# Kernel optimization log

Hardware: AMD Instinct MI355X
Metric: run time of the kernel (lower is better)

The kernel has to match this reference:

```python
import jax, jax.numpy as jnp
import numpy as np

# Module hyperparameters (from init_kwargs)
H, F = 8, 32            # num_heads, attention_filters
RY, RX = 3, 3           # spatial_radius
PH, PW = 2 * RY + 1, 2 * RX + 1
S = PH * PW             # patch_size = 49
HF = H * F


def setup_inputs() -> dict:
    key = jax.random.key(0)
    ks = jax.random.split(key, 6)
    B, Y, X, C = 4, 64, 64, 256
    x = jax.random.normal(ks[0], (B, Y, X, C), jnp.float32)
    # 1x1 conv kernels == dense matrices over the channel dim (no bias)
    Wq = jax.random.normal(ks[1], (C, HF), jnp.float32) / np.sqrt(C)
    Wk = jax.random.normal(ks[2], (C, HF), jnp.float32) / np.sqrt(C)
    Wv = jax.random.normal(ks[3], (C, HF), jnp.float32) / np.sqrt(C)
    Wo = jax.random.normal(ks[4], (HF, C), jnp.float32) / np.sqrt(HF)
    pos_emb = jax.random.normal(ks[5], (S, HF), jnp.float32) * 0.02
    return {"x": x, "Wq": Wq, "Wk": Wk, "Wv": Wv, "Wo": Wo, "pos_emb": pos_emb}


def reference(x, Wq, Wk, Wv, Wo, pos_emb):
    B, Y, X, C = x.shape
    dtype = x.dtype
    # 1x1 conv projections
    Q = x @ Wq                       # (B,Y,X,HF)
    K = x @ Wk
    V = x @ Wv
    # clipped patch centers (borders reuse interior patches)
    cy = jnp.clip(jnp.arange(Y), RY, Y - RY - 1)   # (Y,)
    cx = jnp.clip(jnp.arange(X), RX, X - RX - 1)   # (X,)
    # query relative-position indices within its patch
    qy = jnp.arange(Y) - cy + RY
    qx = jnp.arange(X) - cx + RX
    qidx = qy[:, None] * PW + qx[None, :]          # (Y,X) in [0,S)
    Q = Q + pos_emb[qidx]                          # add query pos embedding (HF)
    Q = Q.reshape(B, Y, X, H, F)
    K = K.reshape(B, Y, X, H, F)
    V = V.reshape(B, Y, X, H, F)
    cy_g, cx_g = jnp.meshgrid(cy, cx, indexing="ij")  # (Y,X)
    scale = jnp.asarray(1.0 / np.sqrt(F), dtype)
    NEG = jnp.asarray(-1e9, dtype)
    m = jnp.full((B, Y, X, H, 1), NEG, dtype)      # running max
    l = jnp.zeros((B, Y, X, H, 1), dtype)          # running sum-exp
    acc = jnp.zeros((B, Y, X, H, F), dtype)        # running value accumulator
    dy_vec = np.arange(-RY, RY + 1)                # within-chunk offsets ('col' mode)
    for dx in range(-RX, RX + 1):                  # chunk loop over columns (7 chunks)
        ny = jnp.clip(cy_g[None, :, :] + dy_vec[:, None, None], 0, Y - 1)  # (PH,Y,X)
        nx = jnp.clip(cx_g[None, :, :] + dx, 0, X - 1)                     # (1,Y,X)
        nx = jnp.broadcast_to(nx, ny.shape)
        sidx = (dy_vec + RY) * PW + (dx + RX)      # (PH,) relative-pos indices
        # gather neighbor K/V: (B,PH,Y,X,H,F)
        Kc = K[:, ny, nx] + pos_emb[sidx].reshape(PH, 1, 1, H, F)
        Vc = V[:, ny, nx]
        sc = jnp.einsum("byxhf,bsyxhf->byxhs", Q, Kc) * scale  # (B,Y,X,H,PH)
        new_m = jnp.maximum(m, sc.max(axis=-1, keepdims=True))
        alpha = jnp.exp(m - new_m)
        p = jnp.exp(sc - new_m)
        l = l * alpha + p.sum(axis=-1, keepdims=True)
        acc = acc * alpha + jnp.einsum("byxhs,bsyxhf->byxhf", p, Vc)
        m = new_m
    out = (acc / (l + 1e-8)).reshape(B, Y, X, HF) @ Wo
    return out
```

## Files before the change

### kernel.cpp

```cpp
#include <hip/hip_runtime.h>
#include <hip/hip_bf16.h>

static constexpr int NPOS = 4 * 64 * 64;
static constexpr int CD   = 256;
#define QSCALE (0.17677669529663687f * 1.4426950408889634f)

typedef __attribute__((ext_vector_type(8))) short bf16x8;
typedef __attribute__((ext_vector_type(4))) float f32x4;

__device__ __forceinline__ float bflo(unsigned int u) { return __uint_as_float(u << 16); }
__device__ __forceinline__ float bfhi(unsigned int u) { return __uint_as_float(u & 0xffff0000u); }

__device__ __forceinline__ unsigned short bfbits(float f) {
    union { __hip_bfloat16 h; unsigned short u; } cv;
    cv.h = __float2bfloat16(f);
    return cv.u;
}
__device__ __forceinline__ unsigned int packbf2(float lo, float hi) {
    union { __hip_bfloat162 h; unsigned int u; } cv;
    cv.h.x = __float2bfloat16(lo);
    cv.h.y = __float2bfloat16(hi);
    return cv.u;
}
__device__ __forceinline__ uint4 pack8(float4 a, float4 b) {
    uint4 u;
    u.x = packbf2(a.x, a.y); u.y = packbf2(a.z, a.w);
    u.z = packbf2(b.x, b.y); u.w = packbf2(b.z, b.w);
    return u;
}
template<int CTRL>
__device__ __forceinline__ float dpp_mov(float v) {
    return __int_as_float(
        __builtin_amdgcn_update_dpp(0, __float_as_int(v), CTRL, 0xF, 0xF, true));
}
template<int IMM>
__device__ __forceinline__ float swz(float v) {
    return __int_as_float(__builtin_amdgcn_ds_swizzle(__float_as_int(v), IMM));
}
__device__ __forceinline__ void async16(void* lds, const void* g) {
    __builtin_amdgcn_global_load_lds(
        (const __attribute__((address_space(1))) unsigned int*)g,
        (__attribute__((address_space(3))) unsigned int*)lds, 16, 0, 0);
}

__global__ __launch_bounds__(256) void convertx_kernel(
    const float* __restrict__ x, unsigned short* __restrict__ xb)
{
    int t = blockIdx.x * 256 + threadIdx.x;
    const float4* s = (const float4*)x + (size_t)t * 2;
    float4 a = s[0], b = s[1];
    ((uint4*)xb)[t] = pack8(a, b);
}

__global__ __launch_bounds__(256) void convert1_kernel(
    const float* __restrict__ Wq, const float* __restrict__ Wk,
    const float* __restrict__ Wv, const float* __restrict__ Wo,
    const float* __restrict__ pe,
    __hip_bfloat16* __restrict__ Wfrag,
    __hip_bfloat16* __restrict__ pebf,
    __hip_bfloat16* __restrict__ Wofrag)
{
    int t = blockIdx.x * 256 + threadIdx.x;
    if (t < 24576) {
        int L = t & 63, ng = (t >> 6) & 7, s = (t >> 9) & 7, T = t >> 12;
        int mat = T >> 1;
        const float* src = (mat == 0) ? Wq : (mat == 1) ? Wk : Wv;
        int ncol  = (T & 1) * 128 + ng * 16 + (L & 15);
        int kbase = s * 32 + (L >> 4) * 8;
        __hip_bfloat16* dst = Wfrag + ((size_t)((T * 8 + s) * 8 + ng) * 64 + L) * 8;
#pragma unroll
        for (int j = 0; j < 8; ++j)
            dst[j] = __float2bfloat16(src[(kbase + j) * 256 + ncol]);
    } else if (t < 26624) {
        int u = t - 24576;
        int L = u & 63, Tn = (u >> 6) & 3, h = u >> 8;
        int s = Tn * 16 + (L & 15);
        int kbase = (L >> 4) * 8;
        __hip_bfloat16* dst = pebf + ((size_t)((h * 4 + Tn) * 64 + L)) * 8;
#pragma unroll
        for (int j = 0; j < 8; ++j) {
            float v = (s < 49) ? pe[s * 256 + h * 32 + kbase + j] * QSCALE : 0.f;
            dst[j] = __float2bfloat16(v);
        }
    } else if (t < 34816) {
        int u = t - 26624;
        int L = u & 63, ng = (u >> 6) & 7, s = (u >> 9) & 7, T = (u >> 12) & 1;
        int ncol  = T * 128 + ng * 16 + (L & 15);
        int kbase = s * 32 + (L >> 4) * 8;
        __hip_bfloat16* dst = Wofrag + ((size_t)((T * 8 + s) * 8 + ng) * 64 + L) * 8;
#pragma unroll
        for (int j = 0; j < 8; ++j)
            dst[j] = __float2bfloat16(Wo[(kbase + j) * 256 + ncol]);
    }
}

__global__ __launch_bounds__(256, 4) void qkv_mfma(
    const unsigned short* __restrict__ xb,
    const __hip_bfloat16* __restrict__ Wfrag,
    const float* __restrict__ pe,
    unsigned short* __restrict__ QA,
    unsigned short* __restrict__ Kd,
    unsigned short* __restrict__ Vt)
{
    __shared__ __align__(16) short As[2][64 * 32];
    const int t = threadIdx.x;
    const int rowbase = blockIdx.x * 64;
    const int g = blockIdx.y;
    const int L = t & 63;
    const int wave = t >> 6;
    const int quad = L >> 4, lrow = L & 15;
    const int T = g * 2 + (wave >> 1);
    const int ngb = (wave & 1) * 4;

    f32x4 acc[4][4];
#pragma unroll
    for (int i = 0; i < 4; ++i)
#pragma unroll
        for (int j = 0; j < 4; ++j) acc[i][j] = (f32x4){0.f, 0.f, 0.f, 0.f};

    const unsigned short* xs = xb + (size_t)(rowbase + (t >> 2)) * CD + (t & 3) * 8;
    short* d0 = &As[0][t * 8];
    short* d1 = &As[1][t * 8];

    async16(d0, xs);
    __syncthreads();

#pragma unroll
    for (int s = 0; s < 8; ++s) {
        if (s < 7) async16((s & 1) ? d0 : d1, xs + (s + 1) * 32);
        bf16x8 bfr[4];
#pragma unroll
        for (int j = 0; j < 4; ++j)
            bfr[j] = *(const bf16x8*)(Wfrag +
                      ((size_t)((T * 8 + s) * 8 + ngb + j) * 64 + L) * 8);
        const short* Ab = As[s & 1];
#pragma unroll
        for (int i = 0; i < 4; ++i) {
            bf16x8 af = *(const bf16x8*)(Ab + (i * 16 + lrow) * 32 + quad * 8);
#pragma unroll
            for (int j = 0; j < 4; ++j)
                acc[i][j] = __builtin_amdgcn_mfma_f32_16x16x32_bf16(af, bfr[j], acc[i][j], 0, 0, 0);
        }
        __syncthreads();
    }

#pragma unroll
    for (int i = 0; i < 4; ++i) {
#pragma unroll
        for (int r = 0; r < 4; ++r) {
            int row = rowbase + i * 16 + quad * 4 + r;
            if (g == 0) {
                int yy = (row >> 6) & 63, xx = row & 63;
                int cy = min(max(yy, 3), 60), cx = min(max(xx, 3), 60);
                int qidx = (yy - cy + 3) * 7 + (xx - cx + 3);
#pragma unroll
                for (int j = 0; j < 4; ++j) {
                    int c = wave * 64 + j * 16 + lrow;
                    QA[(size_t)row * CD + c] = bfbits(acc[i][j][r] + pe[qidx * 256 + c]);
                }
            } else if (g == 1) {
#pragma unroll
                for (int j = 0; j < 4; ++j) {
                    int c = wave * 64 + j * 16 + lrow;
                    Kd[(size_t)row * CD + c] = bfbits(acc[i][j][r] * QSCALE);
                }
            } else {
#pragma unroll
                for (int j = 0; j < 4; ++j) {
                    int c = wave * 64 + j * 16 + lrow;
                    Vt[(size_t)c * 16384 + row + 3] = bfbits(acc[i][j][r]);
                }
            }
        }
    }
}

__global__ __launch_bounds__(256) void attn_mfma(
    unsigned short* QA,
    const unsigned short* __restrict__ Kd,
    const unsigned short* __restrict__ Vt,
    const __hip_bfloat16* __restrict__ pebf)
{
    __shared__ float qpes[4][16 * 64];
    __shared__ __align__(16) unsigned short ps[4][16 * 40];
    const int t = threadIdx.x, w = t >> 6, L = t & 63;
    const int lrow = L & 15, quad = L >> 4;
    const int id = blockIdx.x * 4 + w;
    const int tile = id >> 3, h = id & 7;
    const int pos0 = tile * 16;
    const int x0 = pos0 & 63;
    const int yy = (pos0 >> 6) & 63, bb = pos0 >> 12;
    const int cy = min(max(yy, 3), 60);

    int cxr[4];
#pragma unroll
    for (int r = 0; r < 4; ++r)
        cxr[r] = min(max(x0 + quad * 4 + r, 3), 60) - x0;

    const int kc0 = min(max(x0 - 3 + lrow, 0), 63);
    const int kc1 = min(max(x0 + 13 + lrow, 0), 63);

    const bf16x8 qa = *(const bf16x8*)(QA + (size_t)(pos0 + lrow) * 256 + h * 32 + quad * 8);

    float* qp = qpes[w];
    const f32x4 zero = {0.f, 0.f, 0.f, 0.f};
#pragma unroll
    for (int Tn = 0; Tn < 4; ++Tn) {
        bf16x8 bp = *(const bf16x8*)(pebf + ((size_t)((h * 4 + Tn) * 64 + L)) * 8);
        f32x4 c = __builtin_amdgcn_mfma_f32_16x16x32_bf16(qa, bp, zero, 0, 0, 0);
#pragma unroll
        for (int r = 0; r < 4; ++r)
            qp[(quad * 4 + r) * 64 + Tn * 16 + lrow] = c[r];
    }
    __builtin_amdgcn_s_waitcnt(0xc07f);

    float lacc[4] = {0.f, 0.f, 0.f, 0.f};
    f32x4 o0 = zero, o1 = zero;
    unsigned short* pw = ps[w];
    int rowpos = bb * 4096 + (cy - 3) * 64;

    for (int dy = 0; dy < 7; ++dy, rowpos += 64) {
        const bf16x8 bk0 = *(const bf16x8*)(Kd + (size_t)(rowpos + kc0) * 256 + h * 32 + quad * 8);
        const bf16x8 bk1 = *(const bf16x8*)(Kd + (size_t)(rowpos + kc1) * 256 + h * 32 + quad * 8);
        f32x4 sc0 = __builtin_amdgcn_mfma_f32_16x16x32_bf16(qa, bk0, zero, 0, 0, 0);
        f32x4 sc1 = __builtin_amdgcn_mfma_f32_16x16x32_bf16(qa, bk1, zero, 0, 0, 0);
        const int dy7 = dy * 7;
#pragma unroll
        for (int r = 0; r < 4; ++r) {
            const int i = quad * 4 + r;
            {
                int dx3 = lrow - cxr[r];
                float qpe = qp[i * 64 + dy7 + min(max(dx3, 0), 6)];
                float e = exp2f(sc0[r] + qpe);
                float p = ((unsigned)dx3 <= 6u) ? e : 0.f;
                lacc[r] += p;
                pw[i * 40 + lrow] = bfbits(p);
            }
            {
                int dx3 = 16 + lrow - cxr[r];
                float qpe = qp[i * 64 + dy7 + min(max(dx3, 0), 6)];
                float e = exp2f(sc1[r] + qpe);
                float p = ((unsigned)dx3 <= 6u) ? e : 0.f;
                lacc[r] += p;
                pw[i * 40 + 16 + lrow] = bfbits(p);
            }
        }
        __builtin_amdgcn_s_waitcnt(0xc07f);
        const bf16x8 pa = *(const bf16x8*)(pw + lrow * 40 + quad * 8);
        const bf16x8 bv0 = *(const bf16x8*)(Vt + (size_t)(h * 32 + lrow) * 16384 + rowpos + x0 + quad * 8);
        const bf16x8 bv1 = *(const bf16x8*)(Vt + (size_t)(h * 32 + 16 + lrow) * 16384 + rowpos + x0 + quad * 8);
        o0 = __builtin_amdgcn_mfma_f32_16x16x32_bf16(pa, bv0, o0, 0, 0, 0);
        o1 = __builtin_amdgcn_mfma_f32_16x16x32_bf16(pa, bv1, o1, 0, 0, 0);
    }

#pragma unroll
    for (int r = 0; r < 4; ++r) {
        float v = lacc[r];
        v += dpp_mov<0xB1>(v);
        v += dpp_mov<0x4E>(v);
        v += swz<0x101F>(v);
        v += swz<0x201F>(v);
        const float inv = 1.f / (v + 1e-8f);
        const int row = pos0 + quad * 4 + r;
        QA[(size_t)row * 256 + h * 32 + lrow]      = bfbits(o0[r] * inv);
        QA[(size_t)row * 256 + h * 32 + 16 + lrow] = bfbits(o1[r] * inv);
    }
}

__global__ __launch_bounds__(256, 4) void oproj_mfma(
    const unsigned short* __restrict__ A,
    const __hip_bfloat16* __restrict__ Wofrag,
    float* __restrict__ out)
{
    __shared__ __align__(16) short As[2][32 * 32];
    const int t = threadIdx.x;
    const int rowbase = blockIdx.x * 32;
    const int L = t & 63;
    const int wave = t >> 6;
    const int quad = L >> 4, lrow = L & 15;
    const int T = wave >> 1;
    const int ngb = (wave & 1) * 4;

    f32x4 acc[2][4];
#pragma unroll
    for (int i = 0; i < 2; ++i)
#pragma unroll
        for (int j = 0; j < 4; ++j) acc[i][j] = (f32x4){0.f, 0.f, 0.f, 0.f};

    const unsigned short* asrc = A + (size_t)(rowbase + (t >> 2)) * CD + (t & 3) * 8;
    short* d0 = &As[0][t * 8];
    short* d1 = &As[1][t * 8];

    if (t < 128) async16(d0, asrc);
    __syncthreads();

#pragma unroll
    for (int s = 0; s < 8; ++s) {
        if (s < 7 && t < 128) async16((s & 1) ? d0 : d1, asrc + (s + 1) * 32);
        bf16x8 bfr[4];
#pragma unroll
        for (int j = 0; j < 4; ++j)
            bfr[j] = *(const bf16x8*)(Wofrag +
                      ((size_t)((T * 8 + s) * 8 + ngb + j) * 64 + L) * 8);
        const short* Ab = As[s & 1];
#pragma unroll
        for (int i = 0; i < 2; ++i) {
            bf16x8 af = *(const bf16x8*)(Ab + (i * 16 + lrow) * 32 + quad * 8);
#pragma unroll
            for (int j = 0; j < 4; ++j)
                acc[i][j] = __builtin_amdgcn_mfma_f32_16x16x32_bf16(af, bfr[j], acc[i][j], 0, 0, 0);
        }
        __syncthreads();
    }

#pragma unroll
    for (int i = 0; i < 2; ++i)
#pragma unroll
        for (int r = 0; r < 4; ++r) {
            int row = rowbase + i * 16 + quad * 4 + r;
#pragma unroll
            for (int j = 0; j < 4; ++j) {
                int c = wave * 64 + j * 16 + lrow;
                out[(size_t)row * CD + c] = acc[i][j][r];
            }
        }
}

extern "C" void kernel_launch(void* const* d_in, const int* in_sizes, int n_in,
                              void* d_out, int out_size, void* d_ws, size_t ws_size,
                              hipStream_t stream)
{
    const float* x  = (const float*)d_in[0];
    const float* Wq = (const float*)d_in[1];
    const float* Wk = (const float*)d_in[2];
    const float* Wv = (const float*)d_in[3];
    const float* Wo = (const float*)d_in[4];
    const float* pe = (const float*)d_in[5];
    float* out = (float*)d_out;

    char* ws = (char*)d_ws;
    unsigned short* QA = (unsigned short*)ws;
    unsigned short* Kd = (unsigned short*)(ws + (8u << 20));
    unsigned short* Vt = (unsigned short*)(ws + (16u << 20));
    unsigned short* xb = (unsigned short*)(ws + (24u << 20) + 4096);
    char* fr = ws + (32u << 20) + 8192;
    __hip_bfloat16* Wfrag  = (__hip_bfloat16*)fr;
    __hip_bfloat16* pebf   = (__hip_bfloat16*)(fr + (384u << 10));
    __hip_bfloat16* Wofrag = (__hip_bfloat16*)(fr + (416u << 10));

    convertx_kernel<<<2048, 256, 0, stream>>>(x, xb);
    convert1_kernel<<<136, 256, 0, stream>>>(Wq, Wk, Wv, Wo, pe, Wfrag, pebf, Wofrag);
    qkv_mfma<<<dim3(256, 3), 256, 0, stream>>>(xb, Wfrag, pe, QA, Kd, Vt);
    attn_mfma<<<2048, 256, 0, stream>>>(QA, Kd, Vt, pebf);
    oproj_mfma<<<512, 256, 0, stream>>>(QA, Wofrag, out);
}
```

Before: 138.4 us.

## Merge convert kernels and split V projection with LDS-transposed coalesced stores

Folds the two conversion kernels into one launch. Moves the V projection into its own kernel that stages the transposed output in shared memory, so that Vt writes become contiguous vector stores instead of scattered 2-byte stores. Vt no longer carries a +3 column offset, and the attention kernel's key-window base and V-load offsets shift by 8 to match the new alignment. This trades an extra launch and more LDS use in exchange for coalesced transposed writes.

```diff
diff --git a/kernel.cpp b/kernel.cpp
--- a/kernel.cpp
+++ b/kernel.cpp
@@ -7,9 +7,6 @@
 
 typedef __attribute__((ext_vector_type(8))) short bf16x8;
 typedef __attribute__((ext_vector_type(4))) float f32x4;
-
-__device__ __forceinline__ float bflo(unsigned int u) { return __uint_as_float(u << 16); }
-__device__ __forceinline__ float bfhi(unsigned int u) { return __uint_as_float(u & 0xffff0000u); }
 
 __device__ __forceinline__ unsigned short bfbits(float f) {
     union { __hip_bfloat16 h; unsigned short u; } cv;
@@ -43,16 +40,8 @@
         (__attribute__((address_space(3))) unsigned int*)lds, 16, 0, 0);
 }
 
-__global__ __launch_bounds__(256) void convertx_kernel(
-    const float* __restrict__ x, unsigned short* __restrict__ xb)
-{
-    int t = blockIdx.x * 256 + threadIdx.x;
-    const float4* s = (const float4*)x + (size_t)t * 2;
-    float4 a = s[0], b = s[1];
-    ((uint4*)xb)[t] = pack8(a, b);
-}
-
-__global__ __launch_bounds__(256) void convert1_kernel(
+__global__ __launch_bounds__(256) void convert_kernel(
+    const float* __restrict__ x,  unsigned short* __restrict__ xb,
     const float* __restrict__ Wq, const float* __restrict__ Wk,
     const float* __restrict__ Wv, const float* __restrict__ Wo,
     const float* __restrict__ pe,
@@ -60,6 +49,13 @@
     __hip_bfloat16* __restrict__ pebf,
     __hip_bfloat16* __restrict__ Wofrag)
 {
+    if (blockIdx.x >= 136) {
+        int t = (blockIdx.x - 136) * 256 + threadIdx.x;
+        const float4* s = (const float4*)x + (size_t)t * 2;
+        float4 a = s[0], b = s[1];
+        ((uint4*)xb)[t] = pack8(a, b);
+        return;
+    }
     int t = blockIdx.x * 256 + threadIdx.x;
     if (t < 24576) {
         int L = t & 63, ng = (t >> 6) & 7, s = (t >> 9) & 7, T = t >> 12;
@@ -94,13 +90,12 @@
     }
 }
 
-__global__ __launch_bounds__(256, 4) void qkv_mfma(
+__global__ __launch_bounds__(256, 4) void qk_mfma(
     const unsigned short* __restrict__ xb,
     const __hip_bfloat16* __restrict__ Wfrag,
     const float* __restrict__ pe,
     unsigned short* __restrict__ QA,
-    unsigned short* __restrict__ Kd,
-    unsigned short* __restrict__ Vt)
+    unsigned short* __restrict__ Kd)
 {
     __shared__ __align__(16) short As[2][64 * 32];
     const int t = threadIdx.x;
@@ -158,20 +153,87 @@
                     int c = wave * 64 + j * 16 + lrow;
                     QA[(size_t)row * CD + c] = bfbits(acc[i][j][r] + pe[qidx * 256 + c]);
                 }
-            } else if (g == 1) {
+            } else {
 #pragma unroll
                 for (int j = 0; j < 4; ++j) {
                     int c = wave * 64 + j * 16 + lrow;
                     Kd[(size_t)row * CD + c] = bfbits(acc[i][j][r] * QSCALE);
                 }
-            } else {
-#pragma unroll
-                for (int j = 0; j < 4; ++j) {
-                    int c = wave * 64 + j * 16 + lrow;
-                    Vt[(size_t)c * 16384 + row + 3] = bfbits(acc[i][j][r]);
-                }
             }
         }
+    }
+}
+
+__global__ __launch_bounds__(256, 3) void vproj_mfma(
+    const unsigned short* __restrict__ xb,
+    const __hip_bfloat16* __restrict__ Wfrag,
+    unsigned short* __restrict__ Vt)
+{
+    __shared__ __align__(16) short As[2][64 * 32];
+    __shared__ __align__(8) unsigned short vt[256 * 68];
+    const int t = threadIdx.x;
+    const int rowbase = blockIdx.x * 64;
+    const int L = t & 63;
+    const int wave = t >> 6;
+    const int quad = L >> 4, lrow = L & 15;
+    const int T = 4 + (wave >> 1);
+    const int ngb = (wave & 1) * 4;
+
+    f32x4 acc[4][4];
+#pragma unroll
+    for (int i = 0; i < 4; ++i)
+#pragma unroll
+        for (int j = 0; j < 4; ++j) acc[i][j] = (f32x4){0.f, 0.f, 0.f, 0.f};
+
+    const unsigned short* xs = xb + (size_t)(rowbase + (t >> 2)) * CD + (t & 3) * 8;
+    short* d0 = &As[0][t * 8];
+    short* d1 = &As[1][t * 8];
+
+    async16(d0, xs);
+    __syncthreads();
+
+#pragma unroll
+    for (int s = 0; s < 8; ++s) {
+        if (s < 7) async16((s & 1) ? d0 : d1, xs + (s + 1) * 32);
+        bf16x8 bfr[4];
+#pragma unroll
+        for (int j = 0; j < 4; ++j)
+            bfr[j] = *(const bf16x8*)(Wfrag +
+                      ((size_t)((T * 8 + s) * 8 + ngb + j) * 64 + L) * 8);
+        const short* Ab = As[s & 1];
+#pragma unroll
+        for (int i = 0; i < 4; ++i) {
+            bf16x8 af = *(const bf16x8*)(Ab + (i * 16 + lrow) * 32 + quad * 8);
+#pragma unroll
+            for (int j = 0; j < 4; ++j)
+                acc[i][j] = __builtin_amdgcn_mfma_f32_16x16x32_bf16(af, bfr[j], acc[i][j], 0, 0, 0);
+        }
+        __syncthreads();
+    }
+
+#pragma unroll
+    for (int i = 0; i < 4; ++i) {
+#pragma unroll
+        for (int j = 0; j < 4; ++j) {
+            int c = wave * 64 + j * 16 + lrow;
+            int row0 = i * 16 + quad * 4;
+            *(unsigned int*)&vt[c * 68 + row0] =
+                packbf2(__uint_as_float(0), 0.f),
+            *(unsigned int*)&vt[c * 68 + row0] =
+                (unsigned int)bfbits(acc[i][j][0]) | ((unsigned int)bfbits(acc[i][j][1]) << 16);
+            *(unsigned int*)&vt[c * 68 + row0 + 2] =
+                (unsigned int)bfbits(acc[i][j][2]) | ((unsigned int)bfbits(acc[i][j][3]) << 16);
+        }
+    }
+    __syncthreads();
+
+    const int grp = t >> 4, lig = t & 15;
+    const int row_off = lig * 4;
+#pragma unroll
+    for (int pass = 0; pass < 16; ++pass) {
+        int c = pass * 16 + grp;
+        *(ushort4*)(Vt + (size_t)c * 16384 + rowbase + row_off) =
+            *(const ushort4*)&vt[c * 68 + row_off];
     }
 }
 
@@ -195,10 +257,10 @@
     int cxr[4];
 #pragma unroll
     for (int r = 0; r < 4; ++r)
-        cxr[r] = min(max(x0 + quad * 4 + r, 3), 60) - x0;
-
-    const int kc0 = min(max(x0 - 3 + lrow, 0), 63);
-    const int kc1 = min(max(x0 + 13 + lrow, 0), 63);
+        cxr[r] = min(max(x0 + quad * 4 + r, 3), 60) - x0 + 5;
+
+    const int kc0 = min(max(x0 - 8 + lrow, 0), 63);
+    const int kc1 = min(max(x0 + 8 + lrow, 0), 63);
 
     const bf16x8 qa = *(const bf16x8*)(QA + (size_t)(pos0 + lrow) * 256 + h * 32 + quad * 8);
 
@@ -247,8 +309,8 @@
         }
         __builtin_amdgcn_s_waitcnt(0xc07f);
         const bf16x8 pa = *(const bf16x8*)(pw + lrow * 40 + quad * 8);
-        const bf16x8 bv0 = *(const bf16x8*)(Vt + (size_t)(h * 32 + lrow) * 16384 + rowpos + x0 + quad * 8);
-        const bf16x8 bv1 = *(const bf16x8*)(Vt + (size_t)(h * 32 + 16 + lrow) * 16384 + rowpos + x0 + quad * 8);
+        const bf16x8 bv0 = *(const bf16x8*)(Vt + (size_t)(h * 32 + lrow) * 16384 + rowpos + x0 - 8 + quad * 8);
+        const bf16x8 bv1 = *(const bf16x8*)(Vt + (size_t)(h * 32 + 16 + lrow) * 16384 + rowpos + x0 - 8 + quad * 8);
         o0 = __builtin_amdgcn_mfma_f32_16x16x32_bf16(pa, bv0, o0, 0, 0, 0);
         o1 = __builtin_amdgcn_mfma_f32_16x16x32_bf16(pa, bv1, o1, 0, 0, 0);
     }
@@ -348,9 +410,10 @@
     __hip_bfloat16* pebf   = (__hip_bfloat16*)(fr + (384u << 10));
     __hip_bfloat16* Wofrag = (__hip_bfloat16*)(fr + (416u << 10));
 
-    convertx_kernel<<<2048, 256, 0, stream>>>(x, xb);
-    convert1_kernel<<<136, 256, 0, stream>>>(Wq, Wk, Wv, Wo, pe, Wfrag, pebf, Wofrag);
-    qkv_mfma<<<dim3(256, 3), 256, 0, stream>>>(xb, Wfrag, pe, QA, Kd, Vt);
+    convert_kernel<<<2184, 256, 0, stream>>>(x, xb, Wq, Wk, Wv, Wo, pe,
+                                             Wfrag, pebf, Wofrag);
+    qk_mfma<<<dim3(256, 2), 256, 0, stream>>>(xb, Wfrag, pe, QA, Kd);
+    vproj_mfma<<<256, 256, 0, stream>>>(xb, Wfrag, Vt);
     attn_mfma<<<2048, 256, 0, stream>>>(QA, Kd, Vt, pebf);
     oproj_mfma<<<512, 256, 0, stream>>>(QA, Wofrag, out);
 }
```

New measurement: 138.3 us. About the same (-0.1%).
